# Performance work log

Hardware: AMD Instinct MI355X
Metric: run time of the kernel (lower is better)

Reference implementation:

```python
import jax, jax.numpy as jnp
import numpy as np

B, S, D, H = 8, 1024, 512, 8
DH = D // H


def clinear(x, wr, wi):
    # x: [..., d_in, 2]; wr, wi: [d_out, d_in]
    xr, xi = x[..., 0], x[..., 1]
    yr = xr @ wr.T - xi @ wi.T
    yi = xr @ wi.T + xi @ wr.T
    return jnp.stack((yr, yi), axis=-1)


def split_heads(x):
    # [B, S, D, 2] -> [B, H, S, DH, 2]
    return x.reshape(B, S, H, DH, 2).transpose(0, 2, 1, 3, 4)


def setup_inputs() -> dict:
    key = jax.random.key(0)
    ks = jax.random.split(key, 11)
    std = 1.0 / np.sqrt(D)
    inp = {
        "queries": jax.random.normal(ks[0], (B, S, D, 2), jnp.float32),
        "keys": jax.random.normal(ks[1], (B, S, D, 2), jnp.float32),
        "values": jax.random.normal(ks[2], (B, S, D, 2), jnp.float32),
        "wq_r": jax.random.normal(ks[3], (D, D), jnp.float32) * std,
        "wq_i": jax.random.normal(ks[4], (D, D), jnp.float32) * std,
        "wk_r": jax.random.normal(ks[5], (D, D), jnp.float32) * std,
        "wk_i": jax.random.normal(ks[6], (D, D), jnp.float32) * std,
        "wv_r": jax.random.normal(ks[7], (D, D), jnp.float32) * std,
        "wv_i": jax.random.normal(ks[8], (D, D), jnp.float32) * std,
        "wo_r": jax.random.normal(ks[9], (D, D), jnp.float32) * std,
        "wo_i": jax.random.normal(ks[10], (D, D), jnp.float32) * std,
    }
    return inp


def reference(queries, keys, values, wq_r, wq_i, wk_r, wk_i, wv_r, wv_i, wo_r, wo_i):
    q = split_heads(clinear(queries, wq_r, wq_i))  # [B,H,S,DH,2]
    k = split_heads(clinear(keys, wk_r, wk_i))
    v = split_heads(clinear(values, wv_r, wv_i))
    qr, qi = q[..., 0], q[..., 1]
    kr, ki = k[..., 0], k[..., 1]
    vr, vi = v[..., 0], v[..., 1]
    scale = 1.0 / jnp.sqrt(jnp.asarray(DH, q.dtype))
    # complex QK^T: [B,H,S,S]
    s_r = (jnp.einsum('bhqd,bhkd->bhqk', qr, kr) - jnp.einsum('bhqd,bhkd->bhqk', qi, ki)) * scale
    s_i = (jnp.einsum('bhqd,bhkd->bhqk', qr, ki) + jnp.einsum('bhqd,bhkd->bhqk', qi, kr)) * scale
    a_r = jax.nn.softmax(s_r, axis=-1)
    a_i = jax.nn.softmax(s_i, axis=-1)
    # complex attn @ V (dropout is identity in eval mode)
    o_r = jnp.einsum('bhqk,bhkd->bhqd', a_r, vr) - jnp.einsum('bhqk,bhkd->bhqd', a_i, vi)
    o_i = jnp.einsum('bhqk,bhkd->bhqd', a_r, vi) + jnp.einsum('bhqk,bhkd->bhqd', a_i, vr)
    out = jnp.stack((o_r, o_i), axis=-1)             # [B,H,S,DH,2]
    out = out.transpose(0, 2, 1, 3, 4).reshape(B, S, D, 2)
    return clinear(out, wo_r, wo_i)                  # [B,S,D,2]
```

## Files before the change

kernel.cpp:

```cpp
#include <hip/hip_runtime.h>
#include <cstddef>


typedef __attribute__((ext_vector_type(8))) short bf16x8;
typedef __attribute__((ext_vector_type(4))) float f32x4;

__device__ __forceinline__ unsigned short f2bf(float f) {
  union { float f; unsigned u; } v; v.f = f;
  unsigned r = v.u + 0x7FFFu + ((v.u >> 16) & 1u);
  return (unsigned short)(r >> 16);
}
__device__ __forceinline__ unsigned pk2(float a, float b) {
  return (unsigned)f2bf(a) | ((unsigned)f2bf(b) << 16);
}
__device__ __forceinline__ unsigned pk2t(float a, float b) {
  union { float f; unsigned u; } ua, ub; ua.f = a; ub.f = b;
  return __builtin_amdgcn_perm(ub.u, ua.u, 0x07060302u);
}
__device__ __forceinline__ void gld16(const void* g, void* l) {
  __builtin_amdgcn_global_load_lds(
      (const __attribute__((address_space(1))) unsigned*)g,
      (__attribute__((address_space(3))) unsigned*)l, 16, 0, 0);
}

__global__ __launch_bounds__(256) void prep_weights(
    const float* __restrict__ wq_r, const float* __restrict__ wq_i,
    const float* __restrict__ wk_r, const float* __restrict__ wk_i,
    const float* __restrict__ wv_r, const float* __restrict__ wv_i,
    const float* __restrict__ wo_r, const float* __restrict__ wo_i,
    unsigned* __restrict__ wt) {
  int idx = blockIdx.x * 256 + threadIdx.x;
  int d = idx & 511;
  int n = (idx >> 9) & 1023;
  int p = idx >> 19;
  const float* wr; const float* wi;
  if      (p == 0) { wr = wq_r; wi = wq_i; }
  else if (p == 1) { wr = wk_r; wi = wk_i; }
  else if (p == 2) { wr = wv_r; wi = wv_i; }
  else             { wr = wo_r; wi = wo_i; }
  int j = n >> 1;
  float r = wr[j * 512 + d], im = wi[j * 512 + d];
  unsigned pack = (n & 1) ? pk2(im, r) : pk2(r, -im);
  wt[((size_t)p << 19) + ((size_t)n << 9) + d] = pack;
}

__global__ __launch_bounds__(256) void prep_x(
    const float* __restrict__ xq, const float* __restrict__ xk,
    const float* __restrict__ xv, uint4* __restrict__ xb) {
  int idx = blockIdx.x * 256 + threadIdx.x;
  int p = idx >> 20;
  size_t off = (size_t)(idx & 0xFFFFF) * 8;
  const float* s = (p == 0) ? xq : ((p == 1) ? xk : xv);
  float4 a = *(const float4*)(s + off);
  float4 b = *(const float4*)(s + off + 4);
  xb[idx] = make_uint4(pk2(a.x, a.y), pk2(a.z, a.w),
                       pk2(b.x, b.y), pk2(b.z, b.w));
}

__global__ __launch_bounds__(256) void proj_gemm(
    const unsigned short* __restrict__ xb,
    const unsigned short* __restrict__ wt,
    const unsigned short* __restrict__ aoin,
    unsigned short* __restrict__ qint, unsigned short* __restrict__ kcw,
    unsigned short* __restrict__ vtr, unsigned short* __restrict__ vti,
    float* __restrict__ outp, int mode) {
  __shared__ __align__(16) unsigned short As[128][32];
  __shared__ __align__(16) unsigned short Bs[128][32];
  const int z = (mode == 0) ? blockIdx.z : 3;
  const int tid = threadIdx.x;
  const int m0 = blockIdx.x * 128, n0 = blockIdx.y * 128;
  const int w = tid >> 6, lane = tid & 63;
  const int quad = lane >> 4, l16 = lane & 15;
  const int wm = (w >> 1) * 64, wn = (w & 1) * 64;
  const unsigned short* wtp = wt + ((size_t)z << 20);
  const unsigned short* ax = (mode == 0) ? (xb + ((size_t)z << 23)) : aoin;

  const int rr = lane >> 2;
  const int c8 = (lane & 3) * 8;

  f32x4 acc[4][4];
  #pragma unroll
  for (int i = 0; i < 4; i++)
    #pragma unroll
    for (int j = 0; j < 4; j++) acc[i][j] = (f32x4){0.f, 0.f, 0.f, 0.f};

  for (int k0 = 0; k0 < 1024; k0 += 32) {
    __syncthreads();
    #pragma unroll
    for (int i = 0; i < 2; i++) {
      const int br = (w * 2 + i) * 16;
      gld16(ax  + (size_t)(m0 + br + rr) * 1024 + k0 + c8, (void*)&As[br][0]);
      gld16(wtp + (size_t)(n0 + br + rr) * 1024 + k0 + c8, (void*)&Bs[br][0]);
    }
    __syncthreads();
    bf16x8 af[4], bfr[4];
    #pragma unroll
    for (int mt = 0; mt < 4; mt++)
      af[mt] = *(const bf16x8*)&As[wm + mt * 16 + l16][quad * 8];
    #pragma unroll
    for (int nt = 0; nt < 4; nt++)
      bfr[nt] = *(const bf16x8*)&Bs[wn + nt * 16 + l16][quad * 8];
    #pragma unroll
    for (int mt = 0; mt < 4; mt++)
      #pragma unroll
      for (int nt = 0; nt < 4; nt++)
        acc[mt][nt] = __builtin_amdgcn_mfma_f32_16x16x32_bf16(
            af[mt], bfr[nt], acc[mt][nt], 0, 0, 0);
  }

  #pragma unroll
  for (int mt = 0; mt < 4; mt++) {
    #pragma unroll
    for (int nt = 0; nt < 4; nt++) {
      #pragma unroll
      for (int r = 0; r < 4; r++) {
        int m = m0 + wm + mt * 16 + quad * 4 + r;
        int n = n0 + wn + nt * 16 + l16;
        float v = acc[mt][nt][r];
        if (z == 3) {
          outp[(size_t)m * 1024 + n] = v;
        } else {
          int b = m >> 10, s = m & 1023;
          int h = n >> 7;
          if (z == 0) {
            qint[(((size_t)(b * 8 + h) * 1024 + s) << 7) + (n & 127)] = f2bf(v * 0.125f);
          } else if (z == 1) {
            kcw[(((size_t)(b * 8 + h) * 1024 + s) << 7) + (n & 127)] = f2bf((n & 1) ? -v : v);
          } else {
            int dh = (n >> 1) & 63;
            unsigned short* vp = (n & 1) ? vti : vtr;
            vp[(((size_t)(b * 8 + h) * 64 + dh) << 10) + s] = f2bf(v);
          }
        }
      }
    }
  }
}

__global__ __launch_bounds__(256) void attn_kernel(
    const unsigned short* __restrict__ qint,
    const unsigned short* __restrict__ kcw,
    const unsigned short* __restrict__ vtr,
    const unsigned short* __restrict__ vti,
    unsigned* __restrict__ aout) {
  __shared__ __align__(16) unsigned short Vb[2][2][64][64];
  __shared__ __align__(16) unsigned short Kb[2][64][128];
  __shared__ __align__(16) unsigned short Pb[64][64];
  const int tid = threadIdx.x;
  const int bh = blockIdx.x & 63, qt = blockIdx.x >> 6;
  const int q0 = qt * 64;
  const int w = tid >> 6, lane = tid & 63;
  const int quad = lane >> 4, l16 = lane & 15;
  const unsigned short* qb = qint + (size_t)bh * 1024 * 128;
  const unsigned short* kb = kcw + (size_t)bh * 1024 * 128;
  const unsigned short* vrb = vtr + (size_t)bh * 64 * 1024;
  const unsigned short* vib = vti + (size_t)bh * 64 * 1024;
  const int qrow = w * 16 + l16;
  const int psw = (qrow & 7) << 3;

  const int ri = lane >> 3, oct = lane & 7;
  const int vplane = w >> 1, vrow0 = (w & 1) * 32;
  const unsigned short* vsrc = vplane ? vib : vrb;
  const int osw = (oct ^ ri) * 8;

  const int ri2 = lane >> 4, oct16 = lane & 15;
  const int krsw = (oct16 ^ ri2) * 8;

  bf16x8 qf[4], qs[4];
  #pragma unroll
  for (int kc = 0; kc < 4; kc++) {
    union { bf16x8 v; unsigned u[4]; uint4 q; } a, b;
    a.q = *(const uint4*)(qb + (size_t)(q0 + qrow) * 128 + kc * 32 + quad * 8);
    #pragma unroll
    for (int e = 0; e < 4; e++) {
      unsigned x = a.u[e];
      b.u[e] = ((x >> 16) | (x << 16)) ^ 0x80000000u;
    }
    qf[kc] = a.v; qs[kc] = b.v;
  }

  f32x4 orr[4], ori[4], oir[4], oii[4];
  #pragma unroll
  for (int nt = 0; nt < 4; nt++) {
    orr[nt] = (f32x4){0.f, 0.f, 0.f, 0.f};
    ori[nt] = (f32x4){0.f, 0.f, 0.f, 0.f};
    oir[nt] = (f32x4){0.f, 0.f, 0.f, 0.f};
    oii[nt] = (f32x4){0.f, 0.f, 0.f, 0.f};
  }
  float lr = 0.f, li = 0.f;

  #pragma unroll
  for (int i = 0; i < 4; i++)
    gld16(vsrc + (size_t)(vrow0 + i * 8 + ri) * 1024 + osw,
          (void*)&Vb[0][vplane][vrow0 + i * 8][0]);
  #pragma unroll
  for (int i = 0; i < 4; i++) {
    const int kr = w * 16 + i * 4;
    gld16(kb + (size_t)(kr + ri2) * 128 + (krsw ^ ((i * 4 & 7) * 8)),
          (void*)&Kb[0][kr][0]);
  }
  __syncthreads();

  for (int t = 0; t < 16; t++) {
    const int cur = t & 1;
    const int kp0 = t * 64;
    if (t < 15) {
      #pragma unroll
      for (int i = 0; i < 4; i++)
        gld16(vsrc + (size_t)(vrow0 + i * 8 + ri) * 1024 + (kp0 + 64) + osw,
              (void*)&Vb[1 - cur][vplane][vrow0 + i * 8][0]);
      #pragma unroll
      for (int i = 0; i < 4; i++) {
        const int kr = w * 16 + i * 4;
        gld16(kb + (size_t)(kp0 + 64 + kr + ri2) * 128 + (krsw ^ ((i * 4 & 7) * 8)),
              (void*)&Kb[1 - cur][kr][0]);
      }
    }
    f32x4 sr[4], si[4];
    #pragma unroll
    for (int mt = 0; mt < 4; mt++) {
      sr[mt] = (f32x4){-8.f, -8.f, -8.f, -8.f};
      si[mt] = (f32x4){-8.f, -8.f, -8.f, -8.f};
    }
    #pragma unroll
    for (int mt = 0; mt < 4; mt++) {
      const int krow = mt * 16 + l16;
      #pragma unroll
      for (int kc = 0; kc < 4; kc++) {
        const int slot = ((quad + 4 * kc) ^ (krow & 7)) * 8;
        bf16x8 kf = *(const bf16x8*)&Kb[cur][krow][slot];
        sr[mt] = __builtin_amdgcn_mfma_f32_16x16x32_bf16(kf, qf[kc], sr[mt], 0, 0, 0);
        si[mt] = __builtin_amdgcn_mfma_f32_16x16x32_bf16(kf, qs[kc], si[mt], 0, 0, 0);
      }
    }
    #pragma unroll
    for (int mt = 0; mt < 4; mt++)
      #pragma unroll
      for (int r = 0; r < 4; r++) {
        float pr = __expf(sr[mt][r]);
        float pi = __expf(si[mt][r]);
        sr[mt][r] = pr; si[mt][r] = pi;
        lr += pr; li += pi;
      }
    bf16x8 prf[2], pif[2];
    #pragma unroll
    for (int mt = 0; mt < 4; mt++)
      *(uint2*)&Pb[qrow][(mt * 16 + quad * 4) ^ psw] =
          make_uint2(pk2t(sr[mt][0], sr[mt][1]), pk2t(sr[mt][2], sr[mt][3]));
    #pragma unroll
    for (int kc = 0; kc < 2; kc++)
      prf[kc] = *(const bf16x8*)&Pb[qrow][(kc * 32 + quad * 8) ^ psw];
    #pragma unroll
    for (int mt = 0; mt < 4; mt++)
      *(uint2*)&Pb[qrow][(mt * 16 + quad * 4) ^ psw] =
          make_uint2(pk2t(si[mt][0], si[mt][1]), pk2t(si[mt][2], si[mt][3]));
    #pragma unroll
    for (int kc = 0; kc < 2; kc++)
      pif[kc] = *(const bf16x8*)&Pb[qrow][(kc * 32 + quad * 8) ^ psw];
    #pragma unroll
    for (int kc = 0; kc < 2; kc++) {
      #pragma unroll
      for (int nt = 0; nt < 4; nt++) {
        int dh = nt * 16 + l16;
        int slot = (((kc << 2) + quad) ^ (dh & 7)) * 8;
        bf16x8 vfr = *(const bf16x8*)&Vb[cur][0][dh][slot];
        bf16x8 vfi = *(const bf16x8*)&Vb[cur][1][dh][slot];
        orr[nt] = __builtin_amdgcn_mfma_f32_16x16x32_bf16(prf[kc], vfr, orr[nt], 0, 0, 0);
        ori[nt] = __builtin_amdgcn_mfma_f32_16x16x32_bf16(prf[kc], vfi, ori[nt], 0, 0, 0);
        oir[nt] = __builtin_amdgcn_mfma_f32_16x16x32_bf16(pif[kc], vfr, oir[nt], 0, 0, 0);
        oii[nt] = __builtin_amdgcn_mfma_f32_16x16x32_bf16(pif[kc], vfi, oii[nt], 0, 0, 0);
      }
    }
    __syncthreads();
  }
  lr += __shfl_xor(lr, 16); lr += __shfl_xor(lr, 32);
  li += __shfl_xor(li, 16); li += __shfl_xor(li, 32);
  float lrec = 1.f / lr, irec = 1.f / li;
  float rl[4], il[4];
  #pragma unroll
  for (int r = 0; r < 4; r++) {
    rl[r] = __shfl(lrec, quad * 4 + r);
    il[r] = __shfl(irec, quad * 4 + r);
  }
  const int b = bh >> 3, h = bh & 7;
  #pragma unroll
  for (int nt = 0; nt < 4; nt++) {
    #pragma unroll
    for (int r = 0; r < 4; r++) {
      float o_r = orr[nt][r] * rl[r] - oii[nt][r] * il[r];
      float o_i = ori[nt][r] * rl[r] + oir[nt][r] * il[r];
      int q = q0 + w * 16 + quad * 4 + r;
      int dh = nt * 16 + l16;
      aout[(size_t)(b * 1024 + q) * 512 + (h * 64 + dh)] = pk2(o_r, o_i);
    }
  }
}

extern "C" void kernel_launch(void* const* d_in, const int* in_sizes, int n_in,
                              void* d_out, int out_size, void* d_ws, size_t ws_size,
                              hipStream_t stream) {
  const float* xq = (const float*)d_in[0];
  const float* xk = (const float*)d_in[1];
  const float* xv = (const float*)d_in[2];
  const float* wq_r = (const float*)d_in[3];
  const float* wq_i = (const float*)d_in[4];
  const float* wk_r = (const float*)d_in[5];
  const float* wk_i = (const float*)d_in[6];
  const float* wv_r = (const float*)d_in[7];
  const float* wv_i = (const float*)d_in[8];
  const float* wo_r = (const float*)d_in[9];
  const float* wo_i = (const float*)d_in[10];
  float* outp = (float*)d_out;

  char* ws = (char*)d_ws;
  unsigned short* xb   = (unsigned short*)(ws);
  unsigned short* ao   = (unsigned short*)(ws);
  unsigned short* wt   = (unsigned short*)(ws + ((size_t)48 << 20));
  unsigned short* qint = (unsigned short*)(ws + ((size_t)56 << 20));
  unsigned short* kcw  = (unsigned short*)(ws + ((size_t)72 << 20));
  unsigned short* vtr  = (unsigned short*)(ws + ((size_t)88 << 20));
  unsigned short* vti  = (unsigned short*)(ws + ((size_t)96 << 20));

  prep_weights<<<8192, 256, 0, stream>>>(wq_r, wq_i, wk_r, wk_i, wv_r, wv_i,
                                         wo_r, wo_i, (unsigned*)wt);
  prep_x<<<12288, 256, 0, stream>>>(xq, xk, xv, (uint4*)xb);
  dim3 g1(64, 8, 3);
  proj_gemm<<<g1, 256, 0, stream>>>(xb, wt, ao, qint, kcw, vtr, vti, outp, 0);
  attn_kernel<<<1024, 256, 0, stream>>>(qint, kcw, vtr, vti, (unsigned*)ao);
  dim3 g2(64, 8, 1);
  proj_gemm<<<g2, 256, 0, stream>>>(xb, wt, ao, qint, kcw, vtr, vti, outp, 3);
}
```

Baseline: 364.7 us.

## Merge prep kernels, fold Q scale into input conversion, vectorize projection epilogue

Combines the weight and input bf16 conversion kernels into one launch, saving a launch and letting the two phases overlap. The 1/sqrt(DH) query scale moves from the projection epilogue to the input conversion, where it is exact for a power of two before rounding. The projection epilogue is split per output type: it uses the hardware packed bf16 convert, applies the conjugate sign with an XOR, and writes V-transposed as 8-byte vector stores instead of scalar shorts. Q/K stores stay 2-byte scatters, and the hardware convert may round slightly differently from the software version.

Measured after the change: 343.1 us. 5.9% less time.

```diff
diff --git a/kernel.cpp b/kernel.cpp
--- a/kernel.cpp
+++ b/kernel.cpp
@@ -13,6 +13,11 @@
 __device__ __forceinline__ unsigned pk2(float a, float b) {
   return (unsigned)f2bf(a) | ((unsigned)f2bf(b) << 16);
 }
+__device__ __forceinline__ unsigned cvtpk(float a, float b) {
+  unsigned r;
+  asm("v_cvt_pk_bf16_f32 %0, %1, %2" : "=v"(r) : "v"(a), "v"(b));
+  return r;
+}
 __device__ __forceinline__ unsigned pk2t(float a, float b) {
   union { float f; unsigned u; } ua, ub; ua.f = a; ub.f = b;
   return __builtin_amdgcn_perm(ub.u, ua.u, 0x07060302u);
@@ -23,38 +28,40 @@
       (__attribute__((address_space(3))) unsigned*)l, 16, 0, 0);
 }
 
-__global__ __launch_bounds__(256) void prep_weights(
+__global__ __launch_bounds__(256) void prep_all(
+    const float* __restrict__ xq, const float* __restrict__ xk,
+    const float* __restrict__ xv,
     const float* __restrict__ wq_r, const float* __restrict__ wq_i,
     const float* __restrict__ wk_r, const float* __restrict__ wk_i,
     const float* __restrict__ wv_r, const float* __restrict__ wv_i,
     const float* __restrict__ wo_r, const float* __restrict__ wo_i,
-    unsigned* __restrict__ wt) {
-  int idx = blockIdx.x * 256 + threadIdx.x;
-  int d = idx & 511;
-  int n = (idx >> 9) & 1023;
-  int p = idx >> 19;
-  const float* wr; const float* wi;
-  if      (p == 0) { wr = wq_r; wi = wq_i; }
-  else if (p == 1) { wr = wk_r; wi = wk_i; }
-  else if (p == 2) { wr = wv_r; wi = wv_i; }
-  else             { wr = wo_r; wi = wo_i; }
-  int j = n >> 1;
-  float r = wr[j * 512 + d], im = wi[j * 512 + d];
-  unsigned pack = (n & 1) ? pk2(im, r) : pk2(r, -im);
-  wt[((size_t)p << 19) + ((size_t)n << 9) + d] = pack;
-}
-
-__global__ __launch_bounds__(256) void prep_x(
-    const float* __restrict__ xq, const float* __restrict__ xk,
-    const float* __restrict__ xv, uint4* __restrict__ xb) {
-  int idx = blockIdx.x * 256 + threadIdx.x;
-  int p = idx >> 20;
-  size_t off = (size_t)(idx & 0xFFFFF) * 8;
-  const float* s = (p == 0) ? xq : ((p == 1) ? xk : xv);
-  float4 a = *(const float4*)(s + off);
-  float4 b = *(const float4*)(s + off + 4);
-  xb[idx] = make_uint4(pk2(a.x, a.y), pk2(a.z, a.w),
-                       pk2(b.x, b.y), pk2(b.z, b.w));
+    uint4* __restrict__ xb, unsigned* __restrict__ wt) {
+  const int bid = blockIdx.x;
+  if (bid < 12288) {
+    int idx = bid * 256 + threadIdx.x;
+    int p = idx >> 20;
+    size_t off = (size_t)(idx & 0xFFFFF) * 8;
+    const float* s = (p == 0) ? xq : ((p == 1) ? xk : xv);
+    const float sc = (p == 0) ? 0.125f : 1.0f;
+    float4 a = *(const float4*)(s + off);
+    float4 b = *(const float4*)(s + off + 4);
+    xb[idx] = make_uint4(pk2(sc * a.x, sc * a.y), pk2(sc * a.z, sc * a.w),
+                         pk2(sc * b.x, sc * b.y), pk2(sc * b.z, sc * b.w));
+  } else {
+    int idx = (bid - 12288) * 256 + threadIdx.x;
+    int d = idx & 511;
+    int n = (idx >> 9) & 1023;
+    int p = idx >> 19;
+    const float* wr; const float* wi;
+    if      (p == 0) { wr = wq_r; wi = wq_i; }
+    else if (p == 1) { wr = wk_r; wi = wk_i; }
+    else if (p == 2) { wr = wv_r; wi = wv_i; }
+    else             { wr = wo_r; wi = wo_i; }
+    int j = n >> 1;
+    float r = wr[j * 512 + d], im = wi[j * 512 + d];
+    unsigned pack = (n & 1) ? pk2(im, r) : pk2(r, -im);
+    wt[((size_t)p << 19) + ((size_t)n << 9) + d] = pack;
+  }
 }
 
 __global__ __launch_bounds__(256) void proj_gemm(
@@ -108,30 +115,53 @@
             af[mt], bfr[nt], acc[mt][nt], 0, 0, 0);
   }
 
-  #pragma unroll
-  for (int mt = 0; mt < 4; mt++) {
-    #pragma unroll
-    for (int nt = 0; nt < 4; nt++) {
-      #pragma unroll
-      for (int r = 0; r < 4; r++) {
-        int m = m0 + wm + mt * 16 + quad * 4 + r;
+  const int mbase = m0 + wm + quad * 4;
+  if (z == 3) {
+    #pragma unroll
+    for (int mt = 0; mt < 4; mt++)
+      #pragma unroll
+      for (int nt = 0; nt < 4; nt++)
+        #pragma unroll
+        for (int r = 0; r < 4; r++) {
+          int m = mbase + mt * 16 + r;
+          int n = n0 + wn + nt * 16 + l16;
+          outp[(size_t)m * 1024 + n] = acc[mt][nt][r];
+        }
+  } else if (z == 2) {
+    #pragma unroll
+    for (int mt = 0; mt < 4; mt++) {
+      int m = mbase + mt * 16;
+      int b = m >> 10, s = m & 1023;
+      #pragma unroll
+      for (int nt = 0; nt < 4; nt++) {
         int n = n0 + wn + nt * 16 + l16;
-        float v = acc[mt][nt][r];
-        if (z == 3) {
-          outp[(size_t)m * 1024 + n] = v;
-        } else {
-          int b = m >> 10, s = m & 1023;
-          int h = n >> 7;
-          if (z == 0) {
-            qint[(((size_t)(b * 8 + h) * 1024 + s) << 7) + (n & 127)] = f2bf(v * 0.125f);
-          } else if (z == 1) {
-            kcw[(((size_t)(b * 8 + h) * 1024 + s) << 7) + (n & 127)] = f2bf((n & 1) ? -v : v);
-          } else {
-            int dh = (n >> 1) & 63;
-            unsigned short* vp = (n & 1) ? vti : vtr;
-            vp[(((size_t)(b * 8 + h) * 64 + dh) << 10) + s] = f2bf(v);
-          }
-        }
+        int h = n >> 7, dh = (n >> 1) & 63;
+        unsigned short* vp = (n & 1) ? vti : vtr;
+        unsigned lo = cvtpk(acc[mt][nt][0], acc[mt][nt][1]);
+        unsigned hi = cvtpk(acc[mt][nt][2], acc[mt][nt][3]);
+        *(uint2*)(vp + (((size_t)(b * 8 + h) * 64 + dh) << 10) + s) =
+            make_uint2(lo, hi);
+      }
+    }
+  } else {
+    unsigned short* dst = (z == 0) ? qint : kcw;
+    const unsigned sgn = (z == 1 && (l16 & 1)) ? 0x80008000u : 0u;
+    const int h = n0 >> 7;
+    #pragma unroll
+    for (int mt = 0; mt < 4; mt++) {
+      int m = mbase + mt * 16;
+      int b = m >> 10, s = m & 1023;
+      unsigned short* rp = dst + (((size_t)(b * 8 + h) * 1024 + s) << 7)
+                               + wn + l16;
+      #pragma unroll
+      for (int nt = 0; nt < 4; nt++) {
+        unsigned p01 = cvtpk(acc[mt][nt][0], acc[mt][nt][1]) ^ sgn;
+        unsigned p23 = cvtpk(acc[mt][nt][2], acc[mt][nt][3]) ^ sgn;
+        unsigned short* cp = rp + nt * 16;
+        cp[0]   = (unsigned short)p01;
+        cp[128] = (unsigned short)(p01 >> 16);
+        cp[256] = (unsigned short)p23;
+        cp[384] = (unsigned short)(p23 >> 16);
       }
     }
   }
@@ -321,9 +351,9 @@
   unsigned short* vtr  = (unsigned short*)(ws + ((size_t)88 << 20));
   unsigned short* vti  = (unsigned short*)(ws + ((size_t)96 << 20));
 
-  prep_weights<<<8192, 256, 0, stream>>>(wq_r, wq_i, wk_r, wk_i, wv_r, wv_i,
-                                         wo_r, wo_i, (unsigned*)wt);
-  prep_x<<<12288, 256, 0, stream>>>(xq, xk, xv, (uint4*)xb);
+  prep_all<<<20480, 256, 0, stream>>>(xq, xk, xv, wq_r, wq_i, wk_r, wk_i,
+                                      wv_r, wv_i, wo_r, wo_i,
+                                      (uint4*)xb, (unsigned*)wt);
   dim3 g1(64, 8, 3);
   proj_gemm<<<g1, 256, 0, stream>>>(xb, wt, ao, qint, kcw, vtr, vti, outp, 0);
   attn_kernel<<<1024, 256, 0, stream>>>(qint, kcw, vtr, vti, (unsigned*)ao);
```
